# Kernel tuning notes

Measured on AMD Instinct MI355X. Metric: run time of the kernel, lower is better.

## Reference

```python
import jax, jax.numpy as jnp
import numpy as np

H = 4            # num_attention_heads
EPS_LN = 1e-6    # LayerNorm eps
EPS_IN = 1e-5    # InstanceNorm2d eps (no affine)


def layer_norm(x, g, b):
    m = x.mean(-1, keepdims=True)
    v = ((x - m) ** 2).mean(-1, keepdims=True)
    return (x - m) * jax.lax.rsqrt(v + EPS_LN) * g + b


def instance_norm(s):
    # s: [B,H,C,KV]; InstanceNorm2d(H): normalize per (b,h) over spatial dims (C,KV)
    m = s.mean(axis=(2, 3), keepdims=True)
    v = s.var(axis=(2, 3), keepdims=True)
    return (s - m) * jax.lax.rsqrt(v + EPS_IN)


def _forward(emb1, emb2, emb3, emb4,
             an1_g, an1_b, Wq1, Wo1, fn1_g, fn1_b, fc11_w, fc11_b, fc12_w, fc12_b,
             an2_g, an2_b, Wq2, Wo2, fn2_g, fn2_b, fc21_w, fc21_b, fc22_w, fc22_b,
             an3_g, an3_b, Wq3, Wo3, fn3_g, fn3_b, fc31_w, fc31_b, fc32_w, fc32_b,
             an4_g, an4_b, Wq4, Wo4, fn4_g, fn4_b, fc41_w, fc41_b, fc42_w, fc42_b,
             anA_g, anA_b, Wk, Wv):
    embs = [emb1, emb2, emb3, emb4]
    branches = [
        (an1_g, an1_b, Wq1, Wo1, fn1_g, fn1_b, fc11_w, fc11_b, fc12_w, fc12_b),
        (an2_g, an2_b, Wq2, Wo2, fn2_g, fn2_b, fc21_w, fc21_b, fc22_w, fc22_b),
        (an3_g, an3_b, Wq3, Wo3, fn3_g, fn3_b, fc31_w, fc31_b, fc32_w, fc32_b),
        (an4_g, an4_b, Wq4, Wo4, fn4_g, fn4_b, fc41_w, fc41_b, fc42_w, fc42_b),
    ]
    emb_all = jnp.concatenate(embs, axis=-1)          # [B, n, KV]
    KV = emb_all.shape[-1]
    ea = layer_norm(emb_all, anA_g, anA_b)
    # per-head K/V projections (torch Linear: y = x @ W^T), stacked over heads
    K = jnp.einsum('bnk,hjk->bhnj', ea, Wk)           # [B,H,n,KV]
    V = jnp.einsum('bnk,hjk->bhnj', ea, Wv)           # [B,H,n,KV]
    scale = 1.0 / np.sqrt(KV).astype(np.float32)
    outs = []
    for e, (ag, ab, Wq, Wo, fg, fb, w1, b1, w2, b2) in zip(embs, branches):
        cx = layer_norm(e, ag, ab)                    # [B,n,C]
        Q = jnp.einsum('bnc,hdc->bhnd', cx, Wq)       # [B,H,n,C]
        # channel-attention scores: Q^T K over tokens -> [B,H,C,KV]
        scores = jnp.einsum('bhnd,bhnj->bhdj', Q, K) * scale
        probs = jax.nn.softmax(instance_norm(scores), axis=-1)
        # context [B,H,C,n] averaged over heads -> [B,n,C] (fused into einsum)
        ctx = jnp.einsum('bhdj,bhnj->bnd', probs, V) / H
        O = ctx @ Wo.T                                # out projection
        x = e + O                                     # residual
        h = layer_norm(x, fg, fb)
        h = jax.nn.gelu(h @ w1.T + b1, approximate=False)
        h = h @ w2.T + b2
        outs.append(x + h)                            # FFN residual
    return outs


def setup_inputs() -> dict:
    key = jax.random.key(0)
    B, N = 4, 784
    Cs = [64, 128, 256, 512]
    KV = sum(Cs)
    ks = iter(jax.random.split(key, 64))
    def nrm(shape, scale=0.02):
        return jax.random.normal(next(ks), shape, dtype=jnp.float32) * scale
    inp = {}
    for i, C in enumerate(Cs, 1):
        inp[f'emb{i}'] = jax.random.normal(next(ks), (B, N, C), dtype=jnp.float32)
        inp[f'an{i}_g'] = jnp.ones((C,), jnp.float32)
        inp[f'an{i}_b'] = jnp.zeros((C,), jnp.float32)
        inp[f'Wq{i}'] = nrm((H, C, C))
        inp[f'Wo{i}'] = nrm((C, C))
        inp[f'fn{i}_g'] = jnp.ones((C,), jnp.float32)
        inp[f'fn{i}_b'] = jnp.zeros((C,), jnp.float32)
        inp[f'fc{i}1_w'] = nrm((4 * C, C))
        inp[f'fc{i}1_b'] = nrm((4 * C,), 1e-6)
        inp[f'fc{i}2_w'] = nrm((C, 4 * C))
        inp[f'fc{i}2_b'] = nrm((C,), 1e-6)
    inp['anA_g'] = jnp.ones((KV,), jnp.float32)
    inp['anA_b'] = jnp.zeros((KV,), jnp.float32)
    inp['Wk'] = nrm((H, KV, KV))
    inp['Wv'] = nrm((H, KV, KV))
    return inp


def reference(emb1, emb2, emb3, emb4,
              an1_g, an1_b, Wq1, Wo1, fn1_g, fn1_b, fc11_w, fc11_b, fc12_w, fc12_b,
              an2_g, an2_b, Wq2, Wo2, fn2_g, fn2_b, fc21_w, fc21_b, fc22_w, fc22_b,
              an3_g, an3_b, Wq3, Wo3, fn3_g, fn3_b, fc31_w, fc31_b, fc32_w, fc32_b,
              an4_g, an4_b, Wq4, Wo4, fn4_g, fn4_b, fc41_w, fc41_b, fc42_w, fc42_b,
              anA_g, anA_b, Wk, Wv):
    outs = _forward(emb1, emb2, emb3, emb4,
                    an1_g, an1_b, Wq1, Wo1, fn1_g, fn1_b, fc11_w, fc11_b, fc12_w, fc12_b,
                    an2_g, an2_b, Wq2, Wo2, fn2_g, fn2_b, fc21_w, fc21_b, fc22_w, fc22_b,
                    an3_g, an3_b, Wq3, Wo3, fn3_g, fn3_b, fc31_w, fc31_b, fc32_w, fc32_b,
                    an4_g, an4_b, Wq4, Wo4, fn4_g, fn4_b, fc41_w, fc41_b, fc42_w, fc42_b,
                    anA_g, anA_b, Wk, Wv)
    return tuple(outs)
```

## Files before the change

### kernel.cpp

```cpp
#include <hip/hip_runtime.h>
#include <hip/hip_bf16.h>


using bf16 = __hip_bfloat16;
typedef __attribute__((ext_vector_type(8))) short short8;
typedef __attribute__((ext_vector_type(4))) float f32x4;

__device__ inline float bf2f(unsigned short u) {
    return __uint_as_float(((unsigned int)u) << 16);
}
__device__ inline unsigned short f2b(float f) {
    unsigned int u = __float_as_uint(f);
    return (unsigned short)((u + 0x7fffu + ((u >> 16) & 1u)) >> 16);
}
__device__ inline float ld1f(const float* p) { return *p; }
__device__ inline float ld1f(const bf16* p) { return bf2f(*(const unsigned short*)p); }
__device__ inline void st1(float* p, float v) { *p = v; }
__device__ inline void st1(bf16* p, float v) { *((unsigned short*)p) = f2b(v); }
__device__ inline float4 ld4f(const bf16* p) {
    ushort4 u = *(const ushort4*)p;
    return make_float4(bf2f(u.x), bf2f(u.y), bf2f(u.z), bf2f(u.w));
}

__device__ __forceinline__ void cp16(const void* g, void* l) {
    __builtin_amdgcn_global_load_lds(
        (const __attribute__((address_space(1))) void*)g,
        (__attribute__((address_space(3))) void*)l, 16, 0, 0);
}

__device__ inline float blockSum256(float v, float* red) {
    #pragma unroll
    for (int o = 32; o > 0; o >>= 1) v += __shfl_down(v, o);
    int t = threadIdx.x;
    if ((t & 63) == 0) red[t >> 6] = v;
    __syncthreads();
    float r = red[0] + red[1] + red[2] + red[3];
    __syncthreads();
    return r;
}
__device__ inline float blockMax256(float v, float* red) {
    #pragma unroll
    for (int o = 32; o > 0; o >>= 1) v = fmaxf(v, __shfl_down(v, o));
    int t = threadIdx.x;
    if ((t & 63) == 0) red[t >> 6] = v;
    __syncthreads();
    float r = fmaxf(fmaxf(red[0], red[1]), fmaxf(red[2], red[3]));
    __syncthreads();
    return r;
}

struct CvtN {
    const float* s[18];
    unsigned short* d[18];
    long n[18];
    float* z;
};
__global__ __launch_bounds__(256)
void cvtn_kernel(CvtN a) {
    if (a.z && blockIdx.x == 0 && threadIdx.x < 128) a.z[threadIdx.x] = 0.f;
    long tid = (long)blockIdx.x * 256 + threadIdx.x;
    long stride = (long)gridDim.x * 256;
    for (int g = 0; g < 18; g++) {
        const float* s = a.s[g];
        unsigned short* d = a.d[g];
        long n = a.n[g];
        for (long i = tid * 4; i < n; i += stride * 4) {
            float4 v = *(const float4*)(s + i);
            *(ushort4*)(d + i) = make_ushort4(f2b(v.x), f2b(v.y), f2b(v.z), f2b(v.w));
        }
    }
}

__global__ __launch_bounds__(512, 2)
void mfma8kv(const bf16* __restrict__ A, const bf16* __restrict__ B,
             bf16* __restrict__ KT, bf16* __restrict__ V) {
    __shared__ short Asl[2][2][256][32];
    __shared__ short Bsl[2][2][256][32];
    const int M = 3136, lda = 960, ldb = 960;
    int orig = (int)blockIdx.y * 32 + (int)blockIdx.x;
    int c = orig & 7, r2 = orig >> 3;
    int bx = (c & 3) * 8 + (r2 & 7);
    int by = (c >> 2) * 7 + (r2 >> 3);
    int m0 = by * 256, n0 = bx * 256;
    if (m0 >= M || n0 >= 7680) return;
    int t = threadIdx.x, lane = t & 63, wv = t >> 6;
    int col = lane & 15, quad = lane >> 4;
    int wm = wv >> 2, wn = wv & 3;
    f32x4 acc[8][4];
    #pragma unroll
    for (int i = 0; i < 8; i++)
        #pragma unroll
        for (int j = 0; j < 4; j++) acc[i][j] = (f32x4){0.f, 0.f, 0.f, 0.f};

    int srow = lane >> 2;
    int scol = ((lane & 3) ^ ((lane >> 3) & 3)) << 3;
    int rslot = (quad ^ ((col >> 1) & 3)) << 3;

    auto stageA = [&](int s2, int kt, int kh) {
        int k0 = kt * 64 + kh * 32;
        #pragma unroll
        for (int r = 0; r < 2; r++) {
            int R0 = (r * 8 + wv) * 16;
            cp16(A + (long)(m0 + R0 + srow) * lda + k0 + scol, &Asl[s2][kh][R0][0]);
        }
    };
    auto stageB = [&](int s2, int kt, int kh) {
        int k0 = kt * 64 + kh * 32;
        #pragma unroll
        for (int r = 0; r < 2; r++) {
            int R0 = (r * 8 + wv) * 16;
            cp16(B + (long)(n0 + R0 + srow) * ldb + k0 + scol, &Bsl[s2][kh][R0][0]);
        }
    };

    const int nk = 15;
    stageA(0, 0, 0); stageB(0, 0, 0); stageA(0, 0, 1); stageB(0, 0, 1);
    __syncthreads();

    for (int kt = 0; kt < nk; kt++) {
        int cur = kt & 1, nxt = cur ^ 1;
        bool st = (kt + 1 < nk);
        short8 af[8], bf8[4];
        #pragma unroll
        for (int ni = 0; ni < 4; ni++)
            bf8[ni] = *(const short8*)&Bsl[cur][0][wn * 64 + ni * 16 + col][rslot];
        #pragma unroll
        for (int mi = 0; mi < 4; mi++)
            af[mi] = *(const short8*)&Asl[cur][0][wm * 128 + mi * 16 + col][rslot];
        if (st) stageA(nxt, kt + 1, 0);
        __builtin_amdgcn_s_barrier();
        asm volatile("s_waitcnt lgkmcnt(0)" ::: "memory");
        __builtin_amdgcn_sched_barrier(0);
        __builtin_amdgcn_s_setprio(1);
        #pragma unroll
        for (int mi = 0; mi < 4; mi++)
            #pragma unroll
            for (int ni = 0; ni < 4; ni++)
                acc[mi][ni] = __builtin_amdgcn_mfma_f32_16x16x32_bf16(
                    af[mi], bf8[ni], acc[mi][ni], 0, 0, 0);
        __builtin_amdgcn_s_setprio(0);
        __builtin_amdgcn_s_barrier();
        #pragma unroll
        for (int mi = 4; mi < 8; mi++)
            af[mi] = *(const short8*)&Asl[cur][0][wm * 128 + mi * 16 + col][rslot];
        if (st) stageB(nxt, kt + 1, 0);
        __builtin_amdgcn_s_barrier();
        asm volatile("s_waitcnt lgkmcnt(0)" ::: "memory");
        __builtin_amdgcn_sched_barrier(0);
        __builtin_amdgcn_s_setprio(1);
        #pragma unroll
        for (int mi = 4; mi < 8; mi++)
            #pragma unroll
            for (int ni = 0; ni < 4; ni++)
                acc[mi][ni] = __builtin_amdgcn_mfma_f32_16x16x32_bf16(
                    af[mi], bf8[ni], acc[mi][ni], 0, 0, 0);
        __builtin_amdgcn_s_setprio(0);
        if (st) asm volatile("s_waitcnt vmcnt(4)" ::: "memory");
        else    asm volatile("s_waitcnt vmcnt(0)" ::: "memory");
        __builtin_amdgcn_s_barrier();
        #pragma unroll
        for (int ni = 0; ni < 4; ni++)
            bf8[ni] = *(const short8*)&Bsl[cur][1][wn * 64 + ni * 16 + col][rslot];
        #pragma unroll
        for (int mi = 0; mi < 4; mi++)
            af[mi] = *(const short8*)&Asl[cur][1][wm * 128 + mi * 16 + col][rslot];
        if (st) stageA(nxt, kt + 1, 1);
        __builtin_amdgcn_s_barrier();
        asm volatile("s_waitcnt lgkmcnt(0)" ::: "memory");
        __builtin_amdgcn_sched_barrier(0);
        __builtin_amdgcn_s_setprio(1);
        #pragma unroll
        for (int mi = 0; mi < 4; mi++)
            #pragma unroll
            for (int ni = 0; ni < 4; ni++)
                acc[mi][ni] = __builtin_amdgcn_mfma_f32_16x16x32_bf16(
                    af[mi], bf8[ni], acc[mi][ni], 0, 0, 0);
        __builtin_amdgcn_s_setprio(0);
        __builtin_amdgcn_s_barrier();
        #pragma unroll
        for (int mi = 4; mi < 8; mi++)
            af[mi] = *(const short8*)&Asl[cur][1][wm * 128 + mi * 16 + col][rslot];
        if (st) stageB(nxt, kt + 1, 1);
        __builtin_amdgcn_s_barrier();
        asm volatile("s_waitcnt lgkmcnt(0)" ::: "memory");
        __builtin_amdgcn_sched_barrier(0);
        __builtin_amdgcn_s_setprio(1);
        #pragma unroll
        for (int mi = 4; mi < 8; mi++)
            #pragma unroll
            for (int ni = 0; ni < 4; ni++)
                acc[mi][ni] = __builtin_amdgcn_mfma_f32_16x16x32_bf16(
                    af[mi], bf8[ni], acc[mi][ni], 0, 0, 0);
        __builtin_amdgcn_s_setprio(0);
        if (st) asm volatile("s_waitcnt vmcnt(4)" ::: "memory");
        __builtin_amdgcn_s_barrier();
    }
    #pragma unroll
    for (int mi = 0; mi < 8; mi++) {
        int gmB = m0 + wm * 128 + mi * 16 + quad * 4;
        #pragma unroll
        for (int ni = 0; ni < 4; ni++) {
            int gn = n0 + wn * 64 + ni * 16 + col;
            if (gn < 3840) {
                if (gmB < M) {
                    ushort4 w = make_ushort4(f2b(acc[mi][ni][0]), f2b(acc[mi][ni][1]),
                                             f2b(acc[mi][ni][2]), f2b(acc[mi][ni][3]));
                    *(ushort4*)((unsigned short*)KT + (long)gn * M + gmB) = w;
                }
            } else {
                int vn = gn - 3840;
                #pragma unroll
                for (int r = 0; r < 4; r++) {
                    int gm = gmB + r;
                    if (gm < M) st1(V + (long)gm * 3840 + vn, acc[mi][ni][r]);
                }
            }
        }
    }
}

template <class CT, class RT, bool TO>
__global__ __launch_bounds__(256, 3)
void mfma4(const bf16* __restrict__ A, long Ah, long Ab, int lda,
           const bf16* __restrict__ B, long Bh, long Bb, int ldb,
           CT* __restrict__ Cp, long Ch, long Cb, int ldc,
           const float* __restrict__ bias, const RT* __restrict__ res,
           int M, int N, int K, int Mpad, int Npad, int qx, int hy,
           float alpha, int dogelu, float* __restrict__ stat) {
    __shared__ short Asl[3][128][32];
    __shared__ short Bsl[3][128][32];
    int gx = gridDim.x, gy = gridDim.y;
    int orig = ((int)blockIdx.z * gy + (int)blockIdx.y) * gx + (int)blockIdx.x;
    int bx, by, bz;
    if (qx) {
        int c = orig & 7, r2 = orig >> 3;
        bx = (c & 3) * qx + r2 % qx;
        by = (c >> 2) * hy + r2 / qx;
        bz = 0;
    } else {
        int nxy = gx * gy, nwg = nxy * (int)gridDim.z;
        int q = nwg >> 3, r8 = nwg & 7;
        int xcd = orig & 7, pos = orig >> 3;
        int wgid = (xcd < r8 ? xcd * (q + 1) : r8 * (q + 1) + (xcd - r8) * q) + pos;
        bz = wgid / nxy;
        int rem = wgid - bz * nxy;
        by = rem / gx; bx = rem - by * gx;
    }
    int z = bz;
    A += (long)(z & 3) * Ah + (long)(z >> 2) * Ab;
    B += (long)(z & 3) * Bh + (long)(z >> 2) * Bb;
    Cp += (long)(z & 3) * Ch + (long)(z >> 2) * Cb;
    int m0 = by * 128, n0 = bx * 128;
    int t = threadIdx.x, lane = t & 63, wv = t >> 6;
    int col = lane & 15, quad = lane >> 4;
    int wm = wv >> 1, wn = wv & 1;
    f32x4 acc[4][4];
    #pragma unroll
    for (int i = 0; i < 4; i++)
        #pragma unroll
        for (int j = 0; j < 4; j++) acc[i][j] = (f32x4){0.f, 0.f, 0.f, 0.f};

    const bool fA = (m0 + 128 <= Mpad);
    const bool fB = (n0 + 128 <= Npad);
    int srow = lane >> 2;
    int scol = ((lane & 3) ^ ((lane >> 3) & 3)) << 3;
    int rslot = (quad ^ ((col >> 1) & 3)) << 3;

    auto stageA = [&](int s3, int kt) {
        int k0 = kt * 32;
        if (fA && k0 + 32 <= K) {
            #pragma unroll
            for (int r = 0; r < 2; r++) {
                int R0 = (r * 4 + wv) * 16;
                cp16(A + (long)(m0 + R0 + srow) * lda + k0 + scol, &Asl[s3][R0][0]);
            }
        } else {
            #pragma unroll
            for (int r = 0; r < 2; r++) {
                int idx = r * 256 + t;
                int row = idx >> 2, sl = idx & 3;
                int f2 = (row >> 1) & 3;
                short8 v = {};
                if (m0 + row < M && k0 + sl * 8 < K)
                    v = *(const short8*)(A + (long)(m0 + row) * lda + k0 + sl * 8);
                *(short8*)&Asl[s3][row][(sl ^ f2) * 8] = v;
            }
            asm volatile("s_waitcnt lgkmcnt(0)" ::: "memory");
        }
    };
    auto stageB = [&](int s3, int kt) {
        int k0 = kt * 32;
        if (fB && k0 + 32 <= K) {
            #pragma unroll
            for (int r = 0; r < 2; r++) {
                int R0 = (r * 4 + wv) * 16;
                cp16(B + (long)(n0 + R0 + srow) * ldb + k0 + scol, &Bsl[s3][R0][0]);
            }
        } else {
            #pragma unroll
            for (int r = 0; r < 2; r++) {
                int idx = r * 256 + t;
                int row = idx >> 2, sl = idx & 3;
                int f2 = (row >> 1) & 3;
                short8 v = {};
                if (n0 + row < N && k0 + sl * 8 < K)
                    v = *(const short8*)(B + (long)(n0 + row) * ldb + k0 + sl * 8);
                *(short8*)&Bsl[s3][row][(sl ^ f2) * 8] = v;
            }
            asm volatile("s_waitcnt lgkmcnt(0)" ::: "memory");
        }
    };

    int nk = (K + 31) >> 5;
    stageA(0, 0); stageB(0, 0);
    stageA(1, 1); stageB(1, 1);
    __syncthreads();

    for (int kt = 0; kt < nk; kt++) {
        int cur = kt % 3;
        short8 af[4], bf4[4];
        #pragma unroll
        for (int mi = 0; mi < 4; mi++)
            af[mi] = *(const short8*)&Asl[cur][wm * 64 + mi * 16 + col][rslot];
        #pragma unroll
        for (int ni = 0; ni < 4; ni++)
            bf4[ni] = *(const short8*)&Bsl[cur][wn * 64 + ni * 16 + col][rslot];
        int pend = 0;
        if (kt + 2 < nk) {
            int s3 = (kt + 2) % 3;
            stageA(s3, kt + 2); stageB(s3, kt + 2);
            if ((kt + 2) * 32 + 32 <= K) pend = (fA ? 2 : 0) + (fB ? 2 : 0);
        }
        __builtin_amdgcn_s_barrier();
        asm volatile("s_waitcnt lgkmcnt(0)" ::: "memory");
        __builtin_amdgcn_sched_barrier(0);
        __builtin_amdgcn_s_setprio(1);
        #pragma unroll
        for (int mi = 0; mi < 4; mi++)
            #pragma unroll
            for (int ni = 0; ni < 4; ni++)
                acc[mi][ni] = __builtin_amdgcn_mfma_f32_16x16x32_bf16(
                    af[mi], bf4[ni], acc[mi][ni], 0, 0, 0);
        __builtin_amdgcn_s_setprio(0);
        if (kt + 1 < nk) {
            if (pend == 4)      asm volatile("s_waitcnt vmcnt(4)" ::: "memory");
            else if (pend == 2) asm volatile("s_waitcnt vmcnt(2)" ::: "memory");
            else                asm volatile("s_waitcnt vmcnt(0)" ::: "memory");
            __builtin_amdgcn_s_barrier();
        }
    }
    float psum = 0.f, psq = 0.f;
    #pragma unroll
    for (int mi = 0; mi < 4; mi++) {
        int gmB = m0 + wm * 64 + mi * 16 + quad * 4;
        #pragma unroll
        for (int ni = 0; ni < 4; ni++) {
            int gn = n0 + wn * 64 + ni * 16 + col;
            if constexpr (TO) {
                if (gmB < M && gn < N) {
                    ushort4 w = make_ushort4(f2b(acc[mi][ni][0] * alpha),
                                             f2b(acc[mi][ni][1] * alpha),
                                             f2b(acc[mi][ni][2] * alpha),
                                             f2b(acc[mi][ni][3] * alpha));
                    *(ushort4*)((unsigned short*)Cp + (long)gn * ldc + gmB) = w;
                }
            } else {
                if (gn < N) {
                    float bz2 = bias ? bias[gn] : 0.f;
                    #pragma unroll
                    for (int r = 0; r < 4; r++) {
                        int gm = gmB + r;
                        if (gm < M) {
                            float v = acc[mi][ni][r] * alpha + bz2;
                            if (dogelu) v = 0.5f * v * (1.f + erff(v * 0.70710678118f));
                            if (res) v += ld1f(res + (long)gm * ldc + gn);
                            st1(Cp + (long)gm * ldc + gn, v);
                            psum += v; psq += v * v;
                        }
                    }
                }
            }
        }
    }
    if (stat) {
        __syncthreads();
        #pragma unroll
        for (int o = 32; o > 0; o >>= 1) {
            psum += __shfl_down(psum, o);
            psq  += __shfl_down(psq, o);
        }
        float* red = (float*)Asl;
        if ((t & 63) == 0) { red[wv] = psum; red[4 + wv] = psq; }
        __syncthreads();
        if (t == 0) {
            atomicAdd(&stat[2 * z],     red[0] + red[1] + red[2] + red[3]);
            atomicAdd(&stat[2 * z + 1], red[4] + red[5] + red[6] + red[7]);
        }
    }
}

struct GZ {
    const bf16* A[4]; const bf16* B[4]; bf16* C[4];
    long Ah[4], Ab[4], Bh[4], Bb[4], Ch[4], Cb[4];
    int lda[4], ldb[4], ldc[4], M[4], N[4], K[4], Mpad[4], Npad[4], nbx[4], nby[4];
    float alpha[4];
    float* stat[4];
    int cum[5];
};
template <bool TO>
__global__ __launch_bounds__(256, 3)
void mfmaGZ(GZ g) {
    __shared__ short Asl[3][128][32];
    __shared__ short Bsl[3][128][32];
    int nwg = gridDim.x;
    int orig = blockIdx.x;
    int q = nwg >> 3, r8 = nwg & 7;
    int xcd = orig & 7, pos = orig >> 3;
    int wgid = (xcd < r8 ? xcd * (q + 1) : r8 * (q + 1) + (xcd - r8) * q) + pos;
    int gi = 0;
    if (wgid >= g.cum[1]) gi = 1;
    if (wgid >= g.cum[2]) gi = 2;
    if (wgid >= g.cum[3]) gi = 3;
    int local = wgid - g.cum[gi];
    int nbx = g.nbx[gi], nby = g.nby[gi];
    int z = local / (nbx * nby);
    int rem = local - z * nbx * nby;
    int by = rem / nbx, bx = rem - by * nbx;
    const bf16* A = g.A[gi] + (long)(z & 3) * g.Ah[gi] + (long)(z >> 2) * g.Ab[gi];
    const bf16* B = g.B[gi] + (long)(z & 3) * g.Bh[gi] + (long)(z >> 2) * g.Bb[gi];
    bf16* Cp = g.C[gi] + (long)(z & 3) * g.Ch[gi] + (long)(z >> 2) * g.Cb[gi];
    int lda = g.lda[gi], ldb = g.ldb[gi], ldc = g.ldc[gi];
    int M = g.M[gi], N = g.N[gi], K = g.K[gi];
    int Mpad = g.Mpad[gi], Npad = g.Npad[gi];
    float alpha = g.alpha[gi];
    float* stat = g.stat[gi];

    int m0 = by * 128, n0 = bx * 128;
    int t = threadIdx.x, lane = t & 63, wv = t >> 6;
    int col = lane & 15, quad = lane >> 4;
    int wm = wv >> 1, wn = wv & 1;
    f32x4 acc[4][4];
    #pragma unroll
    for (int i = 0; i < 4; i++)
        #pragma unroll
        for (int j = 0; j < 4; j++) acc[i][j] = (f32x4){0.f, 0.f, 0.f, 0.f};

    const bool fA = (m0 + 128 <= Mpad);
    const bool fB = (n0 + 128 <= Npad);
    int srow = lane >> 2;
    int scol = ((lane & 3) ^ ((lane >> 3) & 3)) << 3;
    int rslot = (quad ^ ((col >> 1) & 3)) << 3;

    auto stageA = [&](int s3, int kt) {
        int k0 = kt * 32;
        if (fA && k0 + 32 <= K) {
            #pragma unroll
            for (int r = 0; r < 2; r++) {
                int R0 = (r * 4 + wv) * 16;
                cp16(A + (long)(m0 + R0 + srow) * lda + k0 + scol, &Asl[s3][R0][0]);
            }
        } else {
            #pragma unroll
            for (int r = 0; r < 2; r++) {
                int idx = r * 256 + t;
                int row = idx >> 2, sl = idx & 3;
                int f2 = (row >> 1) & 3;
                short8 v = {};
                if (m0 + row < M && k0 + sl * 8 < K)
                    v = *(const short8*)(A + (long)(m0 + row) * lda + k0 + sl * 8);
                *(short8*)&Asl[s3][row][(sl ^ f2) * 8] = v;
            }
            asm volatile("s_waitcnt lgkmcnt(0)" ::: "memory");
        }
    };
    auto stageB = [&](int s3, int kt) {
        int k0 = kt * 32;
        if (fB && k0 + 32 <= K) {
            #pragma unroll
            for (int r = 0; r < 2; r++) {
                int R0 = (r * 4 + wv) * 16;
                cp16(B + (long)(n0 + R0 + srow) * ldb + k0 + scol, &Bsl[s3][R0][0]);
            }
        } else {
            #pragma unroll
            for (int r = 0; r < 2; r++) {
                int idx = r * 256 + t;
                int row = idx >> 2, sl = idx & 3;
                int f2 = (row >> 1) & 3;
                short8 v = {};
                if (n0 + row < N && k0 + sl * 8 < K)
                    v = *(const short8*)(B + (long)(n0 + row) * ldb + k0 + sl * 8);
                *(short8*)&Bsl[s3][row][(sl ^ f2) * 8] = v;
            }
            asm volatile("s_waitcnt lgkmcnt(0)" ::: "memory");
        }
    };

    int nk = (K + 31) >> 5;
    stageA(0, 0); stageB(0, 0);
    stageA(1, 1); stageB(1, 1);
    __syncthreads();

    for (int kt = 0; kt < nk; kt++) {
        int cur = kt % 3;
        short8 af[4], bf4[4];
        #pragma unroll
        for (int mi = 0; mi < 4; mi++)
            af[mi] = *(const short8*)&Asl[cur][wm * 64 + mi * 16 + col][rslot];
        #pragma unroll
        for (int ni = 0; ni < 4; ni++)
            bf4[ni] = *(const short8*)&Bsl[cur][wn * 64 + ni * 16 + col][rslot];
        int pend = 0;
        if (kt + 2 < nk) {
            int s3 = (kt + 2) % 3;
            stageA(s3, kt + 2); stageB(s3, kt + 2);
            if ((kt + 2) * 32 + 32 <= K) pend = (fA ? 2 : 0) + (fB ? 2 : 0);
        }
        __builtin_amdgcn_s_barrier();
        asm volatile("s_waitcnt lgkmcnt(0)" ::: "memory");
        __builtin_amdgcn_sched_barrier(0);
        __builtin_amdgcn_s_setprio(1);
        #pragma unroll
        for (int mi = 0; mi < 4; mi++)
            #pragma unroll
            for (int ni = 0; ni < 4; ni++)
                acc[mi][ni] = __builtin_amdgcn_mfma_f32_16x16x32_bf16(
                    af[mi], bf4[ni], acc[mi][ni], 0, 0, 0);
        __builtin_amdgcn_s_setprio(0);
        if (kt + 1 < nk) {
            if (pend == 4)      asm volatile("s_waitcnt vmcnt(4)" ::: "memory");
            else if (pend == 2) asm volatile("s_waitcnt vmcnt(2)" ::: "memory");
            else                asm volatile("s_waitcnt vmcnt(0)" ::: "memory");
            __builtin_amdgcn_s_barrier();
        }
    }
    float psum = 0.f, psq = 0.f;
    #pragma unroll
    for (int mi = 0; mi < 4; mi++) {
        int gmB = m0 + wm * 64 + mi * 16 + quad * 4;
        #pragma unroll
        for (int ni = 0; ni < 4; ni++) {
            int gn = n0 + wn * 64 + ni * 16 + col;
            if constexpr (TO) {
                if (gmB < M && gn < N) {
                    ushort4 w = make_ushort4(f2b(acc[mi][ni][0] * alpha),
                                             f2b(acc[mi][ni][1] * alpha),
                                             f2b(acc[mi][ni][2] * alpha),
                                             f2b(acc[mi][ni][3] * alpha));
                    *(ushort4*)((unsigned short*)Cp + (long)gn * ldc + gmB) = w;
                }
            } else {
                if (gn < N) {
                    #pragma unroll
                    for (int r = 0; r < 4; r++) {
                        int gm = gmB + r;
                        if (gm < M) {
                            float v = acc[mi][ni][r] * alpha;
                            st1(Cp + (long)gm * ldc + gn, v);
                            psum += v; psq += v * v;
                        }
                    }
                }
            }
        }
    }
    if (stat) {
        __syncthreads();
        #pragma unroll
        for (int o = 32; o > 0; o >>= 1) {
            psum += __shfl_down(psum, o);
            psq  += __shfl_down(psq, o);
        }
        float* red = (float*)Asl;
        if ((t & 63) == 0) { red[wv] = psum; red[4 + wv] = psq; }
        __syncthreads();
        if (t == 0) {
            atomicAdd(&stat[2 * z],     red[0] + red[1] + red[2] + red[3]);
            atomicAdd(&stat[2 * z + 1], red[4] + red[5] + red[6] + red[7]);
        }
    }
}

struct G4 {
    const bf16* A[4]; const bf16* B[4]; void* Cv[4];
    const float* bias[4]; const void* res[4];
    int M[4], N[4], K[4], lda[4], ldb[4], ldc[4], nbx[4];
    int cum[5];
};
template <class CT, class RT>
__global__ __launch_bounds__(256, 3)
void mfma4g(G4 gp, int dogelu) {
    __shared__ short Asl[3][128][32];
    __shared__ short Bsl[3][128][32];
    int nwg = gridDim.x;
    int orig = blockIdx.x;
    int q = nwg >> 3, r8 = nwg & 7;
    int xcd = orig & 7, pos = orig >> 3;
    int wgid = (xcd < r8 ? xcd * (q + 1) : r8 * (q + 1) + (xcd - r8) * q) + pos;
    int gi = 0;
    if (wgid >= gp.cum[1]) gi = 1;
    if (wgid >= gp.cum[2]) gi = 2;
    if (wgid >= gp.cum[3]) gi = 3;
    int local = wgid - gp.cum[gi];
    int nbx = gp.nbx[gi];
    int by = local / nbx, bx = local - by * nbx;
    const bf16* A = gp.A[gi];
    const bf16* B = gp.B[gi];
    CT* Cp = (CT*)gp.Cv[gi];
    const float* bias = gp.bias[gi];
    const RT* res = (const RT*)gp.res[gi];
    int M = gp.M[gi], N = gp.N[gi], K = gp.K[gi];
    int lda = gp.lda[gi], ldb = gp.ldb[gi], ldc = gp.ldc[gi];
    int m0 = by * 128, n0 = bx * 128;
    int t = threadIdx.x, lane = t & 63, wv = t >> 6;
    int col = lane & 15, quad = lane >> 4;
    int wm = wv >> 1, wn = wv & 1;
    f32x4 acc[4][4];
    #pragma unroll
    for (int i = 0; i < 4; i++)
        #pragma unroll
        for (int j = 0; j < 4; j++) acc[i][j] = (f32x4){0.f, 0.f, 0.f, 0.f};

    int srow = lane >> 2;
    int scol = ((lane & 3) ^ ((lane >> 3) & 3)) << 3;
    int rslot = (quad ^ ((col >> 1) & 3)) << 3;

    auto stageA = [&](int s3, int kt) {
        int k0 = kt * 32;
        #pragma unroll
        for (int r = 0; r < 2; r++) {
            int R0 = (r * 4 + wv) * 16;
            cp16(A + (long)(m0 + R0 + srow) * lda + k0 + scol, &Asl[s3][R0][0]);
        }
    };
    auto stageB = [&](int s3, int kt) {
        int k0 = kt * 32;
        #pragma unroll
        for (int r = 0; r < 2; r++) {
            int R0 = (r * 4 + wv) * 16;
            cp16(B + (long)(n0 + R0 + srow) * ldb + k0 + scol, &Bsl[s3][R0][0]);
        }
    };

    int nk = K >> 5;
    stageA(0, 0); stageB(0, 0);
    stageA(1, 1); stageB(1, 1);
    __syncthreads();

    for (int kt = 0; kt < nk; kt++) {
        int cur = kt % 3;
        short8 af[4], bf4[4];
        #pragma unroll
        for (int mi = 0; mi < 4; mi++)
            af[mi] = *(const short8*)&Asl[cur][wm * 64 + mi * 16 + col][rslot];
        #pragma unroll
        for (int ni = 0; ni < 4; ni++)
            bf4[ni] = *(const short8*)&Bsl[cur][wn * 64 + ni * 16 + col][rslot];
        bool st = (kt + 2 < nk);
        if (st) {
            int s3 = (kt + 2) % 3;
            stageA(s3, kt + 2); stageB(s3, kt + 2);
        }
        __builtin_amdgcn_s_barrier();
        asm volatile("s_waitcnt lgkmcnt(0)" ::: "memory");
        __builtin_amdgcn_sched_barrier(0);
        __builtin_amdgcn_s_setprio(1);
        #pragma unroll
        for (int mi = 0; mi < 4; mi++)
            #pragma unroll
            for (int ni = 0; ni < 4; ni++)
                acc[mi][ni] = __builtin_amdgcn_mfma_f32_16x16x32_bf16(
                    af[mi], bf4[ni], acc[mi][ni], 0, 0, 0);
        __builtin_amdgcn_s_setprio(0);
        if (kt + 1 < nk) {
            if (st) asm volatile("s_waitcnt vmcnt(4)" ::: "memory");
            else    asm volatile("s_waitcnt vmcnt(0)" ::: "memory");
            __builtin_amdgcn_s_barrier();
        }
    }
    #pragma unroll
    for (int mi = 0; mi < 4; mi++) {
        int gmB = m0 + wm * 64 + mi * 16 + quad * 4;
        #pragma unroll
        for (int ni = 0; ni < 4; ni++) {
            int gn = n0 + wn * 64 + ni * 16 + col;
            if (gn < N) {
                float bz2 = bias ? bias[gn] : 0.f;
                #pragma unroll
                for (int r = 0; r < 4; r++) {
                    int gm = gmB + r;
                    if (gm < M) {
                        float v = acc[mi][ni][r] + bz2;
                        if (dogelu) v = 0.5f * v * (1.f + erff(v * 0.70710678118f));
                        if (res) v += ld1f(res + (long)gm * ldc + gn);
                        st1(Cp + (long)gm * ldc + gn, v);
                    }
                }
            }
        }
    }
}

struct LNA {
    const float* e[4];
    const float* ag[4];
    const float* ab[4];
    const float* cg;
    const float* cbb;
    bf16* y[4];
    bf16* ea;
};
__global__ __launch_bounds__(256)
void ln_all_kernel(LNA a) {
    __shared__ float x[960];
    __shared__ float red[4];
    long row = blockIdx.x;
    int t = threadIdx.x;
    const int off[5] = {0, 64, 192, 448, 960};
    {
        const float* p1 = a.e[0] + row * 64;
        const float* p2 = a.e[1] + row * 128;
        const float* p3 = a.e[2] + row * 256;
        const float* p4 = a.e[3] + row * 512;
        if (t < 64) x[t] = p1[t];
        for (int i = t; i < 128; i += 256) x[64 + i]  = p2[i];
        for (int i = t; i < 256; i += 256) x[192 + i] = p3[i];
        for (int i = t; i < 512; i += 256) x[448 + i] = p4[i];
    }
    __syncthreads();
    float ssum[4], ssq[4];
    #pragma unroll
    for (int br = 0; br < 4; br++) {
        float s = 0.f, q = 0.f;
        for (int i = off[br] + t; i < off[br + 1]; i += 256) {
            float v = x[i]; s += v; q += v * v;
        }
        ssum[br] = blockSum256(s, red);
        ssq[br]  = blockSum256(q, red);
    }
    float S1 = ssum[0] + ssum[1] + ssum[2] + ssum[3];
    float S2 = ssq[0] + ssq[1] + ssq[2] + ssq[3];
    float muA = S1 * (1.f / 960.f);
    float rA = rsqrtf(S2 * (1.f / 960.f) - muA * muA + 1e-6f);
    for (int i = t; i < 960; i += 256)
        st1(a.ea + row * 960 + i, (x[i] - muA) * rA * a.cg[i] + a.cbb[i]);
    #pragma unroll
    for (int br = 0; br < 4; br++) {
        int C = off[br + 1] - off[br];
        float mu = ssum[br] / C;
        float rr = rsqrtf(ssq[br] / C - mu * mu + 1e-6f);
        const float* g = a.ag[br];
        const float* b = a.ab[br];
        bf16* y = a.y[br] + row * C;
        for (int i = t; i < C; i += 256)
            st1(y + i, (x[off[br] + i] - mu) * rr * g[i] + b[i]);
    }
}

struct LR4 {
    const bf16* X[4];
    const float* g[4];
    const float* b[4];
    bf16* Y[4];
    int C[4];
};
__global__ __launch_bounds__(256)
void ln_rows4_kernel(LR4 a) {
    __shared__ float x[512];
    __shared__ float red[4];
    int br = blockIdx.y;
    long row = blockIdx.x;
    int C = a.C[br];
    int t = threadIdx.x;
    const bf16* xr = a.X[br] + row * C;
    float s = 0.f, q = 0.f;
    for (int i = t; i < C; i += 256) { float v = ld1f(xr + i); x[i] = v; s += v; q += v * v; }
    float S1 = blockSum256(s, red), S2 = blockSum256(q, red);
    float mu = S1 / C;
    float r = rsqrtf(S2 / C - mu * mu + 1e-6f);
    const float* g = a.g[br];
    const float* b = a.b[br];
    bf16* y = a.Y[br] + row * C;
    for (int i = t; i < C; i += 256)
        st1(y + i, (x[i] - mu) * r * g[i] + b[i]);
}

struct SMX {
    bf16* S[4];
    const float* stat[4];
    int C[4];
    int cum[5];
};
__global__ __launch_bounds__(256)
void softmax_all_kernel(SMX a) {
    __shared__ float x[960];
    __shared__ float red[4];
    int rid = blockIdx.x;
    int gi = 0;
    if (rid >= a.cum[1]) gi = 1;
    if (rid >= a.cum[2]) gi = 2;
    if (rid >= a.cum[3]) gi = 3;
    int local = rid - a.cum[gi];
    int C = a.C[gi];
    int z = local / C;
    int d = local - z * C;
    int t = threadIdx.x;
    float n = 960.f * (float)C;
    float s0 = a.stat[gi][2 * z], q0 = a.stat[gi][2 * z + 1];
    float mu = s0 / n;
    float rs = rsqrtf(q0 / n - mu * mu + 1e-5f);
    int h = z & 3, b = z >> 2;
    bf16* row = a.S[gi] + (long)b * C * 3840 + (long)d * 3840 + h * 960;
    float mx = -3.4e38f;
    for (int i = t; i < 960; i += 256) {
        float v = ld1f(row + i) * rs; x[i] = v; mx = fmaxf(mx, v);
    }
    float M = blockMax256(mx, red);
    float s = 0.f;
    for (int i = t; i < 960; i += 256) { float e = __expf(x[i] - M); x[i] = e; s += e; }
    float Ssum = blockSum256(s, red);
    float inv = 1.f / Ssum;
    for (int i = t; i < 960; i += 256) st1(row + i, x[i] * inv);
}

struct CSX {
    const bf16* tmp[4];
    bf16* ctx[4];
    long NTC[4];
    int cum[5];
};
__global__ __launch_bounds__(256)
void ctxsum_all_kernel(CSX a) {
    int bid = blockIdx.x;
    int gi = 0;
    if (bid >= a.cum[1]) gi = 1;
    if (bid >= a.cum[2]) gi = 2;
    if (bid >= a.cum[3]) gi = 3;
    long local = bid - a.cum[gi];
    long NTC = a.NTC[gi];
    const bf16* tmp = a.tmp[gi];
    long i = (local * 256 + threadIdx.x) * 4;
    float4 p = ld4f(tmp + i);
    float4 b = ld4f(tmp + NTC + i);
    float4 c = ld4f(tmp + 2 * NTC + i);
    float4 d = ld4f(tmp + 3 * NTC + i);
    ushort4 o = make_ushort4(f2b((p.x + b.x + c.x + d.x) * 0.25f),
                             f2b((p.y + b.y + c.y + d.y) * 0.25f),
                             f2b((p.z + b.z + c.z + d.z) * 0.25f),
                             f2b((p.w + b.w + c.w + d.w) * 0.25f));
    *(ushort4*)(a.ctx[gi] + i) = o;
}

extern "C" void kernel_launch(void* const* d_in, const int* in_sizes, int n_in,
                              void* d_out, int out_size, void* d_ws, size_t ws_size,
                              hipStream_t stream) {
    (void)in_sizes; (void)n_in; (void)out_size; (void)ws_size;
    const int Cs[4] = {64, 128, 256, 512};
    const float *emb[4], *ang[4], *anb[4], *Wq[4], *Wo[4], *fng[4], *fnb[4], *w1[4], *b1[4], *w2[4], *b2[4];
    for (int i = 0; i < 4; i++) {
        const int base = i * 11;
        emb[i] = (const float*)d_in[base + 0];
        ang[i] = (const float*)d_in[base + 1];
        anb[i] = (const float*)d_in[base + 2];
        Wq[i]  = (const float*)d_in[base + 3];
        Wo[i]  = (const float*)d_in[base + 4];
        fng[i] = (const float*)d_in[base + 5];
        fnb[i] = (const float*)d_in[base + 6];
        w1[i]  = (const float*)d_in[base + 7];
        b1[i]  = (const float*)d_in[base + 8];
        w2[i]  = (const float*)d_in[base + 9];
        b2[i]  = (const float*)d_in[base + 10];
    }
    const float* anAg = (const float*)d_in[44];
    const float* anAb = (const float*)d_in[45];
    const float* Wk   = (const float*)d_in[46];
    const float* Wv   = (const float*)d_in[47];

    const int NT = 3136;
    char* wsb = (char*)d_ws;
    unsigned short* wp = (unsigned short*)(wsb);
    float* statb = (float*)(wsb + 9052160);
    bf16*  KT    = (bf16*)(wsb + 9053184);
    bf16*  tmpb  = KT;
    bf16*  hid   = KT;
    bf16*  Vb2   = (bf16*)(wsb + 33137664);
    bf16*  cx2   = (bf16*)(wsb + 33137664);
    bf16*  xball = (bf16*)(wsb + 39158784);
    bf16*  cx3   = (bf16*)(wsb + 45179904);
    bf16*  QTp   = (bf16*)(wsb + 57222144);
    bf16*  wkv   = (bf16*)(wsb + 57222144);
    bf16*  S5    = (bf16*)(wsb + 70067200);
    bf16*  ea    = (bf16*)(wsb + 71967744);
    bf16*  SR    = (bf16*)(wsb + 85795840);
    bf16*  cxall = (bf16*)(wsb + 85795840);

    const long wb[4]  = {0, 53248, 266240, 1118208};
    const long co[4]  = {0, 200704, 602112, 1404928};
    const long ho[4]  = {0, 802816, 2408448, 5619712};
    const long qro[3] = {4816896, 3211264, 0};
    const long sro[3] = {5898240, 3932160, 0};
    const long tpo[4] = {11239424, 9633792, 6422528, 0};

    float* out = (float*)d_out;
    const float scale = 0.03227486121f;

    {
        CvtN a;
        a.s[0] = Wk; a.d[0] = (unsigned short*)wkv;           a.n[0] = 3686400;
        a.s[1] = Wv; a.d[1] = (unsigned short*)wkv + 3686400; a.n[1] = 3686400;
        for (int i = 0; i < 4; i++) {
            const long C2 = (long)Cs[i] * Cs[i];
            a.s[2 + 4 * i] = Wq[i]; a.d[2 + 4 * i] = wp + wb[i];          a.n[2 + 4 * i] = 4 * C2;
            a.s[3 + 4 * i] = Wo[i]; a.d[3 + 4 * i] = wp + wb[i] + 4 * C2; a.n[3 + 4 * i] = C2;
            a.s[4 + 4 * i] = w1[i]; a.d[4 + 4 * i] = wp + wb[i] + 5 * C2; a.n[4 + 4 * i] = 4 * C2;
            a.s[5 + 4 * i] = w2[i]; a.d[5 + 4 * i] = wp + wb[i] + 9 * C2; a.n[5 + 4 * i] = 4 * C2;
        }
        a.z = statb;
        cvtn_kernel<<<1024, 256, 0, stream>>>(a);
    }
    {
        LNA a;
        for (int i = 0; i < 4; i++) {
            a.e[i] = emb[i]; a.ag[i] = ang[i]; a.ab[i] = anb[i];
            a.y[i] = cxall + co[i];
        }
        a.cg = anAg; a.cbb = anAb; a.ea = ea;
        ln_all_kernel<<<3136, 256, 0, stream>>>(a);
    }
    mfma8kv<<<dim3(32, 14, 1), 512, 0, stream>>>(ea, wkv, KT, Vb2);

    mfma4<bf16, float, true><<<dim3(4, 26, 4), 256, 0, stream>>>(
        cxall + co[3], 0, 0, 512, (const bf16*)(wp + wb[3]), 262144, 0, 512,
        QTp, 512L * NT, 0, NT,
        nullptr, (const float*)nullptr, NT, 512, 512, 3328, 512, 0, 0,
        1.f, 0, nullptr);
    mfma4<bf16, float, false><<<dim3(8, 4, 16), 256, 0, stream>>>(
        QTp, 512L * NT, 784, NT, KT, 3010560, 784, NT,
        S5, 960, 512L * 3840, 3840,
        nullptr, (const float*)nullptr, 512, 960, 784, 512, 1024, 0, 0,
        scale, 0, statb + 32 * 3);
    {
        GZ g;
        int cum = 0;
        const int ord[3] = {2, 1, 0};
        for (int j = 0; j < 3; j++) {
            int i = ord[j], C = Cs[i];
            g.A[j] = cxall + co[i]; g.Ah[j] = 0; g.Ab[j] = 0; g.lda[j] = C;
            g.B[j] = (const bf16*)(wp + wb[i]); g.Bh[j] = (long)C * C; g.Bb[j] = 0; g.ldb[j] = C;
            g.C[j] = QTp + qro[i]; g.Ch[j] = (long)C * NT; g.Cb[j] = 0; g.ldc[j] = NT;
            g.M[j] = NT; g.N[j] = C; g.K[j] = C;
            g.Mpad[j] = 3328; g.Npad[j] = (C >= 128) ? C : 64;
            g.nbx[j] = (C >= 128) ? C / 128 : 1; g.nby[j] = 26;
            g.alpha[j] = 1.f; g.stat[j] = nullptr;
            g.cum[j] = cum; cum += g.nbx[j] * 26 * 4;
        }
        g.cum[3] = cum; g.cum[4] = cum;
        mfmaGZ<true><<<cum, 256, 0, stream>>>(g);
    }
    {
        GZ g;
        int cum = 0;
        const int ord[3] = {2, 1, 0};
        for (int j = 0; j < 3; j++) {
            int i = ord[j], C = Cs[i];
            g.A[j] = QTp + qro[i]; g.Ah[j] = (long)C * NT; g.Ab[j] = 784; g.lda[j] = NT;
            g.B[j] = KT; g.Bh[j] = 3010560; g.Bb[j] = 784; g.ldb[j] = NT;
            g.C[j] = SR + sro[i]; g.Ch[j] = 960; g.Cb[j] = (long)C * 3840; g.ldc[j] = 3840;
            g.M[j] = C; g.N[j] = 960; g.K[j] = 784;
            g.Mpad[j] = (C >= 128) ? C : 64; g.Npad[j] = 1024;
            g.nbx[j] = 8; g.nby[j] = (C >= 128) ? C / 128 : 1;
            g.alpha[j] = scale; g.stat[j] = statb + 32 * i;
            g.cum[j] = cum; cum += 8 * g.nby[j] * 16;
        }
        g.cum[3] = cum; g.cum[4] = cum;
        mfmaGZ<false><<<cum, 256, 0, stream>>>(g);
    }
    {
        SMX a;
        const int ord[4] = {3, 2, 1, 0};
        int cum = 0;
        for (int j = 0; j < 4; j++) {
            int i = ord[j], C = Cs[i];
            a.S[j] = (i == 3) ? S5 : SR + sro[i];
            a.stat[j] = statb + 32 * i;
            a.C[j] = C;
            a.cum[j] = cum; cum += 16 * C;
        }
        a.cum[4] = cum;
        softmax_all_kernel<<<cum, 256, 0, stream>>>(a);
    }
    {
        GZ g;
        int cum = 0;
        const int ord[4] = {3, 2, 1, 0};
        for (int j = 0; j < 4; j++) {
            int i = ord[j], C = Cs[i];
            g.A[j] = Vb2; g.Ah[j] = 960; g.Ab[j] = 784L * 3840; g.lda[j] = 3840;
            g.B[j] = (i == 3) ? S5 : SR + sro[i];
            g.Bh[j] = 960; g.Bb[j] = (long)C * 3840; g.ldb[j] = 3840;
            g.C[j] = tmpb + tpo[i]; g.Ch[j] = (long)NT * C; g.Cb[j] = 784L * C; g.ldc[j] = C;
            g.M[j] = 784; g.N[j] = C; g.K[j] = 960;
            g.Mpad[j] = 896; g.Npad[j] = (C >= 128) ? C : 64;
            g.nbx[j] = (C >= 128) ? C / 128 : 1; g.nby[j] = 7;
            g.alpha[j] = 1.f; g.stat[j] = nullptr;
            g.cum[j] = cum; cum += g.nbx[j] * 7 * 16;
        }
        g.cum[4] = cum;
        mfmaGZ<false><<<cum, 256, 0, stream>>>(g);
    }
    {
        CSX a;
        int cum = 0;
        const int ord[4] = {3, 2, 1, 0};
        for (int j = 0; j < 4; j++) {
            int i = ord[j], C = Cs[i];
            a.tmp[j] = tmpb + tpo[i]; a.ctx[j] = cx2 + co[i];
            a.NTC[j] = (long)NT * C;
            a.cum[j] = cum; cum += (int)(((long)NT * C) / 1024);
        }
        a.cum[4] = cum;
        ctxsum_all_kernel<<<cum, 256, 0, stream>>>(a);
    }
    {
        G4 g;
        int cum = 0;
        for (int i = 0; i < 4; i++) {
            const int C = Cs[i];
            const long C2 = (long)C * C;
            g.A[i] = cx2 + co[i]; g.B[i] = (const bf16*)(wp + wb[i] + 4 * C2);
            g.Cv[i] = xball + co[i];
            g.bias[i] = nullptr; g.res[i] = emb[i];
            g.M[i] = NT; g.N[i] = C; g.K[i] = C;
            g.lda[i] = C; g.ldb[i] = C; g.ldc[i] = C;
            g.nbx[i] = (C >= 128) ? C / 128 : 1;
            g.cum[i] = cum; cum += g.nbx[i] * 26;
        }
        g.cum[4] = cum;
        mfma4g<bf16, float><<<cum, 256, 0, stream>>>(g, 0);
    }
    {
        LR4 a;
        for (int i = 0; i < 4; i++) {
            a.X[i] = xball + co[i]; a.g[i] = fng[i]; a.b[i] = fnb[i];
            a.Y[i] = cx3 + co[i]; a.C[i] = Cs[i];
        }
        ln_rows4_kernel<<<dim3(3136, 4), 256, 0, stream>>>(a);
    }
    {
        G4 g;
        int cum = 0;
        for (int i = 0; i < 4; i++) {
            const int C = Cs[i];
            const long C2 = (long)C * C;
            g.A[i] = cx3 + co[i]; g.B[i] = (const bf16*)(wp + wb[i] + 5 * C2);
            g.Cv[i] = hid + ho[i];
            g.bias[i] = b1[i]; g.res[i] = nullptr;
            g.M[i] = NT; g.N[i] = 4 * C; g.K[i] = C;
            g.lda[i] = C; g.ldb[i] = C; g.ldc[i] = 4 * C;
            g.nbx[i] = 4 * C / 128;
            g.cum[i] = cum; cum += g.nbx[i] * 26;
        }
        g.cum[4] = cum;
        mfma4g<bf16, float><<<cum, 256, 0, stream>>>(g, 1);
    }
    {
        G4 g;
        int cum = 0;
        for (int i = 0; i < 4; i++) {
            const int C = Cs[i];
            const long C2 = (long)C * C;
            g.A[i] = hid + ho[i]; g.B[i] = (const bf16*)(wp + wb[i] + 9 * C2);
            g.Cv[i] = out + co[i];
            g.bias[i] = b2[i]; g.res[i] = xball + co[i];
            g.M[i] = NT; g.N[i] = C; g.K[i] = 4 * C;
            g.lda[i] = 4 * C; g.ldb[i] = 4 * C; g.ldc[i] = C;
            g.nbx[i] = (C >= 128) ? C / 128 : 1;
            g.cum[i] = cum; cum += g.nbx[i] * 26;
        }
        g.cum[4] = cum;
        mfma4g<float, bf16><<<cum, 256, 0, stream>>>(g, 0);
    }
}
```

Baseline: 632.3 us.

## Fold head-average into context GEMM K-dim and merge weight-convert with LayerNorm

The context GEMM now contracts over all four heads at once (K=3840) with alpha 0.25, writing the head-averaged context directly. This removes the per-head temporary buffer and the separate ctxsum reduction kernel. The weight conversion and input LayerNorm kernels are also merged into one launch using a block-index split. The trade-off is fewer GEMM blocks, each with a four-times-longer K loop, so there is less parallelism per launch. Workspace buffers are remapped to match.

```diff
diff --git a/kernel.cpp b/kernel.cpp
--- a/kernel.cpp
+++ b/kernel.cpp
@@ -55,19 +55,77 @@
     long n[18];
     float* z;
 };
+struct LNA {
+    const float* e[4];
+    const float* ag[4];
+    const float* ab[4];
+    const float* cg;
+    const float* cbb;
+    bf16* y[4];
+    bf16* ea;
+};
+struct Prep { CvtN cv; LNA ln; };
 __global__ __launch_bounds__(256)
-void cvtn_kernel(CvtN a) {
-    if (a.z && blockIdx.x == 0 && threadIdx.x < 128) a.z[threadIdx.x] = 0.f;
-    long tid = (long)blockIdx.x * 256 + threadIdx.x;
-    long stride = (long)gridDim.x * 256;
-    for (int g = 0; g < 18; g++) {
-        const float* s = a.s[g];
-        unsigned short* d = a.d[g];
-        long n = a.n[g];
-        for (long i = tid * 4; i < n; i += stride * 4) {
-            float4 v = *(const float4*)(s + i);
-            *(ushort4*)(d + i) = make_ushort4(f2b(v.x), f2b(v.y), f2b(v.z), f2b(v.w));
-        }
+void prep_kernel(Prep p) {
+    __shared__ float x[960];
+    __shared__ float red[4];
+    if (blockIdx.x < 1024) {
+        CvtN& a = p.cv;
+        if (a.z && blockIdx.x == 0 && threadIdx.x < 128) a.z[threadIdx.x] = 0.f;
+        long tid = (long)blockIdx.x * 256 + threadIdx.x;
+        long stride = 1024L * 256;
+        for (int g = 0; g < 18; g++) {
+            const float* s = a.s[g];
+            unsigned short* d = a.d[g];
+            long n = a.n[g];
+            for (long i = tid * 4; i < n; i += stride * 4) {
+                float4 v = *(const float4*)(s + i);
+                *(ushort4*)(d + i) = make_ushort4(f2b(v.x), f2b(v.y), f2b(v.z), f2b(v.w));
+            }
+        }
+        return;
+    }
+    LNA& a = p.ln;
+    long row = blockIdx.x - 1024;
+    int t = threadIdx.x;
+    const int off[5] = {0, 64, 192, 448, 960};
+    {
+        const float* p1 = a.e[0] + row * 64;
+        const float* p2 = a.e[1] + row * 128;
+        const float* p3 = a.e[2] + row * 256;
+        const float* p4 = a.e[3] + row * 512;
+        if (t < 64) x[t] = p1[t];
+        for (int i = t; i < 128; i += 256) x[64 + i]  = p2[i];
+        for (int i = t; i < 256; i += 256) x[192 + i] = p3[i];
+        for (int i = t; i < 512; i += 256) x[448 + i] = p4[i];
+    }
+    __syncthreads();
+    float ssum[4], ssq[4];
+    #pragma unroll
+    for (int br = 0; br < 4; br++) {
+        float s = 0.f, q = 0.f;
+        for (int i = off[br] + t; i < off[br + 1]; i += 256) {
+            float v = x[i]; s += v; q += v * v;
+        }
+        ssum[br] = blockSum256(s, red);
+        ssq[br]  = blockSum256(q, red);
+    }
+    float S1 = ssum[0] + ssum[1] + ssum[2] + ssum[3];
+    float S2 = ssq[0] + ssq[1] + ssq[2] + ssq[3];
+    float muA = S1 * (1.f / 960.f);
+    float rA = rsqrtf(S2 * (1.f / 960.f) - muA * muA + 1e-6f);
+    for (int i = t; i < 960; i += 256)
+        st1(a.ea + row * 960 + i, (x[i] - muA) * rA * a.cg[i] + a.cbb[i]);
+    #pragma unroll
+    for (int br = 0; br < 4; br++) {
+        int C = off[br + 1] - off[br];
+        float mu = ssum[br] / C;
+        float rr = rsqrtf(ssq[br] / C - mu * mu + 1e-6f);
+        const float* g = a.ag[br];
+        const float* b = a.ab[br];
+        bf16* y = a.y[br] + row * C;
+        for (int i = t; i < C; i += 256)
+            st1(y + i, (x[off[br] + i] - mu) * rr * g[i] + b[i]);
     }
 }
 
@@ -701,62 +759,6 @@
     }
 }
 
-struct LNA {
-    const float* e[4];
-    const float* ag[4];
-    const float* ab[4];
-    const float* cg;
-    const float* cbb;
-    bf16* y[4];
-    bf16* ea;
-};
-__global__ __launch_bounds__(256)
-void ln_all_kernel(LNA a) {
-    __shared__ float x[960];
-    __shared__ float red[4];
-    long row = blockIdx.x;
-    int t = threadIdx.x;
-    const int off[5] = {0, 64, 192, 448, 960};
-    {
-        const float* p1 = a.e[0] + row * 64;
-        const float* p2 = a.e[1] + row * 128;
-        const float* p3 = a.e[2] + row * 256;
-        const float* p4 = a.e[3] + row * 512;
-        if (t < 64) x[t] = p1[t];
-        for (int i = t; i < 128; i += 256) x[64 + i]  = p2[i];
-        for (int i = t; i < 256; i += 256) x[192 + i] = p3[i];
-        for (int i = t; i < 512; i += 256) x[448 + i] = p4[i];
-    }
-    __syncthreads();
-    float ssum[4], ssq[4];
-    #pragma unroll
-    for (int br = 0; br < 4; br++) {
-        float s = 0.f, q = 0.f;
-        for (int i = off[br] + t; i < off[br + 1]; i += 256) {
-            float v = x[i]; s += v; q += v * v;
-        }
-        ssum[br] = blockSum256(s, red);
-        ssq[br]  = blockSum256(q, red);
-    }
-    float S1 = ssum[0] + ssum[1] + ssum[2] + ssum[3];
-    float S2 = ssq[0] + ssq[1] + ssq[2] + ssq[3];
-    float muA = S1 * (1.f / 960.f);
-    float rA = rsqrtf(S2 * (1.f / 960.f) - muA * muA + 1e-6f);
-    for (int i = t; i < 960; i += 256)
-        st1(a.ea + row * 960 + i, (x[i] - muA) * rA * a.cg[i] + a.cbb[i]);
-    #pragma unroll
-    for (int br = 0; br < 4; br++) {
-        int C = off[br + 1] - off[br];
-        float mu = ssum[br] / C;
-        float rr = rsqrtf(ssq[br] / C - mu * mu + 1e-6f);
-        const float* g = a.ag[br];
-        const float* b = a.ab[br];
-        bf16* y = a.y[br] + row * C;
-        for (int i = t; i < C; i += 256)
-            st1(y + i, (x[off[br] + i] - mu) * rr * g[i] + b[i]);
-    }
-}
-
 struct LR4 {
     const bf16* X[4];
     const float* g[4];
@@ -823,34 +825,6 @@
     for (int i = t; i < 960; i += 256) st1(row + i, x[i] * inv);
 }
 
-struct CSX {
-    const bf16* tmp[4];
-    bf16* ctx[4];
-    long NTC[4];
-    int cum[5];
-};
-__global__ __launch_bounds__(256)
-void ctxsum_all_kernel(CSX a) {
-    int bid = blockIdx.x;
-    int gi = 0;
-    if (bid >= a.cum[1]) gi = 1;
-    if (bid >= a.cum[2]) gi = 2;
-    if (bid >= a.cum[3]) gi = 3;
-    long local = bid - a.cum[gi];
-    long NTC = a.NTC[gi];
-    const bf16* tmp = a.tmp[gi];
-    long i = (local * 256 + threadIdx.x) * 4;
-    float4 p = ld4f(tmp + i);
-    float4 b = ld4f(tmp + NTC + i);
-    float4 c = ld4f(tmp + 2 * NTC + i);
-    float4 d = ld4f(tmp + 3 * NTC + i);
-    ushort4 o = make_ushort4(f2b((p.x + b.x + c.x + d.x) * 0.25f),
-                             f2b((p.y + b.y + c.y + d.y) * 0.25f),
-                             f2b((p.z + b.z + c.z + d.z) * 0.25f),
-                             f2b((p.w + b.w + c.w + d.w) * 0.25f));
-    *(ushort4*)(a.ctx[gi] + i) = o;
-}
-
 extern "C" void kernel_launch(void* const* d_in, const int* in_sizes, int n_in,
                               void* d_out, int out_size, void* d_ws, size_t ws_size,
                               hipStream_t stream) {
@@ -881,14 +855,13 @@
     unsigned short* wp = (unsigned short*)(wsb);
     float* statb = (float*)(wsb + 9052160);
     bf16*  KT    = (bf16*)(wsb + 9053184);
-    bf16*  tmpb  = KT;
     bf16*  hid   = KT;
     bf16*  Vb2   = (bf16*)(wsb + 33137664);
-    bf16*  cx2   = (bf16*)(wsb + 33137664);
-    bf16*  xball = (bf16*)(wsb + 39158784);
-    bf16*  cx3   = (bf16*)(wsb + 45179904);
+    bf16*  xball = (bf16*)(wsb + 33137664);
+    bf16*  cx3   = (bf16*)(wsb + 39158784);
     bf16*  QTp   = (bf16*)(wsb + 57222144);
     bf16*  wkv   = (bf16*)(wsb + 57222144);
+    bf16*  cx2   = (bf16*)(wsb + 57222144);
     bf16*  S5    = (bf16*)(wsb + 70067200);
     bf16*  ea    = (bf16*)(wsb + 71967744);
     bf16*  SR    = (bf16*)(wsb + 85795840);
@@ -899,33 +872,28 @@
     const long ho[4]  = {0, 802816, 2408448, 5619712};
     const long qro[3] = {4816896, 3211264, 0};
     const long sro[3] = {5898240, 3932160, 0};
-    const long tpo[4] = {11239424, 9633792, 6422528, 0};
 
     float* out = (float*)d_out;
     const float scale = 0.03227486121f;
 
     {
-        CvtN a;
-        a.s[0] = Wk; a.d[0] = (unsigned short*)wkv;           a.n[0] = 3686400;
-        a.s[1] = Wv; a.d[1] = (unsigned short*)wkv + 3686400; a.n[1] = 3686400;
+        Prep p;
+        p.cv.s[0] = Wk; p.cv.d[0] = (unsigned short*)wkv;           p.cv.n[0] = 3686400;
+        p.cv.s[1] = Wv; p.cv.d[1] = (unsigned short*)wkv + 3686400; p.cv.n[1] = 3686400;
         for (int i = 0; i < 4; i++) {
             const long C2 = (long)Cs[i] * Cs[i];
-            a.s[2 + 4 * i] = Wq[i]; a.d[2 + 4 * i] = wp + wb[i];          a.n[2 + 4 * i] = 4 * C2;
-            a.s[3 + 4 * i] = Wo[i]; a.d[3 + 4 * i] = wp + wb[i] + 4 * C2; a.n[3 + 4 * i] = C2;
-            a.s[4 + 4 * i] = w1[i]; a.d[4 + 4 * i] = wp + wb[i] + 5 * C2; a.n[4 + 4 * i] = 4 * C2;
-            a.s[5 + 4 * i] = w2[i]; a.d[5 + 4 * i] = wp + wb[i] + 9 * C2; a.n[5 + 4 * i] = 4 * C2;
-        }
-        a.z = statb;
-        cvtn_kernel<<<1024, 256, 0, stream>>>(a);
-    }
-    {
-        LNA a;
+            p.cv.s[2 + 4 * i] = Wq[i]; p.cv.d[2 + 4 * i] = wp + wb[i];          p.cv.n[2 + 4 * i] = 4 * C2;
+            p.cv.s[3 + 4 * i] = Wo[i]; p.cv.d[3 + 4 * i] = wp + wb[i] + 4 * C2; p.cv.n[3 + 4 * i] = C2;
+            p.cv.s[4 + 4 * i] = w1[i]; p.cv.d[4 + 4 * i] = wp + wb[i] + 5 * C2; p.cv.n[4 + 4 * i] = 4 * C2;
+            p.cv.s[5 + 4 * i] = w2[i]; p.cv.d[5 + 4 * i] = wp + wb[i] + 9 * C2; p.cv.n[5 + 4 * i] = 4 * C2;
+        }
+        p.cv.z = statb;
         for (int i = 0; i < 4; i++) {
-            a.e[i] = emb[i]; a.ag[i] = ang[i]; a.ab[i] = anb[i];
-            a.y[i] = cxall + co[i];
-        }
-        a.cg = anAg; a.cbb = anAb; a.ea = ea;
-        ln_all_kernel<<<3136, 256, 0, stream>>>(a);
+            p.ln.e[i] = emb[i]; p.ln.ag[i] = ang[i]; p.ln.ab[i] = anb[i];
+            p.ln.y[i] = cxall + co[i];
+        }
+        p.ln.cg = anAg; p.ln.cbb = anAb; p.ln.ea = ea;
+        prep_kernel<<<4160, 256, 0, stream>>>(p);
     }
     mfma8kv<<<dim3(32, 14, 1), 512, 0, stream>>>(ea, wkv, KT, Vb2);
 
@@ -995,31 +963,18 @@
         const int ord[4] = {3, 2, 1, 0};
         for (int j = 0; j < 4; j++) {
             int i = ord[j], C = Cs[i];
-            g.A[j] = Vb2; g.Ah[j] = 960; g.Ab[j] = 784L * 3840; g.lda[j] = 3840;
+            g.A[j] = Vb2; g.Ah[j] = 784L * 3840; g.Ab[j] = 0; g.lda[j] = 3840;
             g.B[j] = (i == 3) ? S5 : SR + sro[i];
-            g.Bh[j] = 960; g.Bb[j] = (long)C * 3840; g.ldb[j] = 3840;
-            g.C[j] = tmpb + tpo[i]; g.Ch[j] = (long)NT * C; g.Cb[j] = 784L * C; g.ldc[j] = C;
-            g.M[j] = 784; g.N[j] = C; g.K[j] = 960;
+            g.Bh[j] = (long)C * 3840; g.Bb[j] = 0; g.ldb[j] = 3840;
+            g.C[j] = cx2 + co[i]; g.Ch[j] = 784L * C; g.Cb[j] = 0; g.ldc[j] = C;
+            g.M[j] = 784; g.N[j] = C; g.K[j] = 3840;
             g.Mpad[j] = 896; g.Npad[j] = (C >= 128) ? C : 64;
             g.nbx[j] = (C >= 128) ? C / 128 : 1; g.nby[j] = 7;
-            g.alpha[j] = 1.f; g.stat[j] = nullptr;
-            g.cum[j] = cum; cum += g.nbx[j] * 7 * 16;
+            g.alpha[j] = 0.25f; g.stat[j] = nullptr;
+            g.cum[j] = cum; cum += g.nbx[j] * 7 * 4;
         }
         g.cum[4] = cum;
         mfmaGZ<false><<<cum, 256, 0, stream>>>(g);
-    }
-    {
-        CSX a;
-        int cum = 0;
-        const int ord[4] = {3, 2, 1, 0};
-        for (int j = 0; j < 4; j++) {
-            int i = ord[j], C = Cs[i];
-            a.tmp[j] = tmpb + tpo[i]; a.ctx[j] = cx2 + co[i];
-            a.NTC[j] = (long)NT * C;
-            a.cum[j] = cum; cum += (int)(((long)NT * C) / 1024);
-        }
-        a.cum[4] = cum;
-        ctxsum_all_kernel<<<cum, 256, 0, stream>>>(a);
     }
     {
         G4 g;
```

After: 644.7 us. About the same (+2.0%).
